# Kernel tuning notes

Hardware: AMD Instinct MI355X
Metric: run time of the kernel (lower is better)

## Reference

```python
import jax, jax.numpy as jnp
import numpy as np
from jax import lax


def _conv(x, w, b, pad):
    # x: [B,C,H,W], w: [O,I,kh,kw]
    y = lax.conv_general_dilated(x, w, (1, 1), [(pad, pad), (pad, pad)],
                                 dimension_numbers=('NCHW', 'OIHW', 'NCHW'))
    return y + b[None, :, None, None]


def _maxpool2(x):
    return lax.reduce_window(x, -jnp.inf, lax.max, (1, 1, 2, 2), (1, 1, 2, 2), 'VALID')


def setup_inputs() -> dict:
    key = jax.random.key(0)
    ks = jax.random.split(key, 6)
    N, T, R, D = 8, 64, 9, 512
    x = jax.random.normal(ks[0], (N, T, R, D), dtype=jnp.float32)
    x = x / jnp.linalg.norm(x, axis=-1, keepdims=True)  # ViSiL features are L2-normalized
    w1 = jax.random.normal(ks[1], (32, 1, 3, 3), dtype=jnp.float32) * 0.05
    w2 = jax.random.normal(ks[2], (64, 32, 3, 3), dtype=jnp.float32) * 0.05
    w3 = jax.random.normal(ks[3], (128, 64, 3, 3), dtype=jnp.float32) * 0.05
    w4 = jax.random.normal(ks[4], (1, 128, 1, 1), dtype=jnp.float32) * 0.05
    return {
        'x': x,
        'w1': w1, 'b1': jnp.zeros((32,), jnp.float32),
        'w2': w2, 'b2': jnp.zeros((64,), jnp.float32),
        'w3': w3, 'b3': jnp.zeros((128,), jnp.float32),
        'w4': w4, 'b4': jnp.zeros((1,), jnp.float32),
    }


def reference(x, w1, b1, w2, b2, w3, b3, w4, b4):
    N, T, R, D = x.shape
    # frame-to-frame similarity: region correlation volume + chamfer (max over p, mean over o)
    sim = jnp.einsum('aiok,bjpk->aiopjb', x, x)        # [a,i,o,p,j,b]
    sim = jnp.mean(jnp.max(sim, axis=3), axis=2)        # [a,i,j,b]
    sim = jnp.transpose(sim, (0, 3, 1, 2)).reshape(N * N, 1, T, T)  # '(a b) () i j'
    # VideoComparator CNN head (ZeroPad2d(1) + valid 3x3 conv == 'same' 3x3 conv)
    h = jax.nn.relu(_conv(sim, w1, b1, 1))
    h = _maxpool2(h)
    h = jax.nn.relu(_conv(h, w2, b2, 1))
    h = _maxpool2(h)
    h = jax.nn.relu(_conv(h, w3, b3, 1))
    h = _conv(h, w4, b4, 0)                              # [N*N, 1, T/4, T/4]
    # SimilarityRegularizationLoss(min_val=-1, max_val=1)
    loss = jnp.sum(jax.nn.relu(-(h + 1.0))) + jnp.sum(jax.nn.relu(h - 1.0))
    # Hardtanh, rescale to [0,1], then video-to-video chamfer
    s = jnp.clip(h, -1.0, 1.0) / 2.0 + 0.5
    s = jnp.mean(jnp.max(s, axis=3), axis=2)             # [N*N, 1]
    return s.reshape(N, N), loss
```

## Files before the change

### kernel.cpp

```cpp
#include <hip/hip_runtime.h>

typedef unsigned short u16;
typedef unsigned int u32;
typedef __bf16 bf16x8 __attribute__((ext_vector_type(8)));
typedef u16 u16x8 __attribute__((ext_vector_type(8)));
typedef float f32x4 __attribute__((ext_vector_type(4)));

__device__ __forceinline__ u16 f2bf(float f) {
  u32 u = __float_as_uint(f);
  u32 r = (u + 0x7FFFu + ((u >> 16) & 1u)) >> 16;
  return (u16)r;
}

__device__ __forceinline__ void gload16(const void* g, void* l) {
  typedef __attribute__((address_space(1))) const void gvoid;
  typedef __attribute__((address_space(3))) void lvoid;
  __builtin_amdgcn_global_load_lds((gvoid*)g, (lvoid*)l, 16, 0, 0);
}

__global__ void k_cast(const float* __restrict__ x, u16* __restrict__ A) {
  int t = blockIdx.x * 256 + threadIdx.x;
  const float4* xp = (const float4*)x + (size_t)t * 2;
  float4 v0 = xp[0], v1 = xp[1];
  u16x8 r;
  r[0] = f2bf(v0.x); r[1] = f2bf(v0.y); r[2] = f2bf(v0.z); r[3] = f2bf(v0.w);
  r[4] = f2bf(v1.x); r[5] = f2bf(v1.y); r[6] = f2bf(v1.z); r[7] = f2bf(v1.w);
  *(u16x8*)(A + (size_t)t * 8) = r;
}

__global__ __launch_bounds__(256) void k_gemm_smax(const u16* __restrict__ A,
                                                   float* __restrict__ Smax,
                                                   float* __restrict__ Sx) {
  __shared__ char smem[33536];
  const int rb = blockIdx.x, cb = blockIdx.y;
  if (rb > cb) return;
  u16* As = (u16*)smem;
  u16* Bs = (u16*)(smem + 16384);
  float* slab = (float*)smem;
  const int rowBase = rb * 128, colBase = cb * 128;
  const int tid = threadIdx.x, wave = tid >> 6, lane = tid & 63;
  const int lr = lane >> 3, lc = lane & 7;
  const int lrow = lane & 15, lk = lane >> 4;
  const int xr = lrow & 7;
  const int wr = (wave & 1) * 64, wc = (wave >> 1) * 64;

  f32x4 acc[4][4];
#pragma unroll
  for (int rt = 0; rt < 4; ++rt)
#pragma unroll
    for (int ct = 0; ct < 4; ++ct) { f32x4 z = {0.f, 0.f, 0.f, 0.f}; acc[rt][ct] = z; }

  for (int k0 = 0; k0 < 512; k0 += 64) {
    __syncthreads();
#pragma unroll
    for (int ii = 0; ii < 4; ++ii) {
      int r0 = wave * 32 + ii * 8;
      gload16(A + (size_t)(rowBase + r0 + lr) * 512 + k0 + ((lc ^ lr) * 8),
              As + r0 * 64);
      gload16(A + (size_t)(colBase + r0 + lr) * 512 + k0 + ((lc ^ lr) * 8),
              Bs + r0 * 64);
    }
    __syncthreads();
#pragma unroll
    for (int s = 0; s < 2; ++s) {
      bf16x8 af[4], bf[4];
#pragma unroll
      for (int rt = 0; rt < 4; ++rt)
        af[rt] = *(const bf16x8*)(As + (wr + rt * 16 + lrow) * 64 +
                                  ((u32)(s * 4 + lk) ^ xr) * 8);
#pragma unroll
      for (int ct = 0; ct < 4; ++ct)
        bf[ct] = *(const bf16x8*)(Bs + (wc + ct * 16 + lrow) * 64 +
                                  ((u32)(s * 4 + lk) ^ xr) * 8);
#pragma unroll
      for (int rt = 0; rt < 4; ++rt)
#pragma unroll
        for (int ct = 0; ct < 4; ++ct)
          acc[rt][ct] = __builtin_amdgcn_mfma_f32_16x16x32_bf16(af[rt], bf[ct],
                                                                acc[rt][ct], 0, 0, 0);
    }
  }

  const int g0c = colBase / 9, offc = colBase % 9;
  const int g0r = rowBase / 9, offr = rowBase % 9;
  const int nph = (rb == cb) ? 2 : 4;
  for (int ph = 0; ph < nph; ++ph) {
    __syncthreads();
    if (ph < 2) {
      if ((wave & 1) == ph) {
#pragma unroll
        for (int rt = 0; rt < 4; ++rt)
#pragma unroll
          for (int ct = 0; ct < 4; ++ct)
#pragma unroll
            for (int r = 0; r < 4; ++r)
              slab[(rt * 16 + lk * 4 + r) * 129 + wc + ct * 16 + lrow] = acc[rt][ct][r];
      }
    } else {
      if ((wave >> 1) == ph - 2) {
#pragma unroll
        for (int rt = 0; rt < 4; ++rt)
#pragma unroll
          for (int ct = 0; ct < 4; ++ct)
#pragma unroll
            for (int r = 0; r < 4; ++r)
              slab[(ct * 16 + lrow) * 129 + wr + rt * 16 + lk * 4 + r] = acc[rt][ct][r];
      }
    }
    __syncthreads();
    for (int it = tid; it < 1024; it += 256) {
      int line = it >> 4, s = it & 15;
      float m = -3.0e38f;
      if (ph < 2) {
        int g = g0c + s;
        int cs = 9 * g - colBase, ce = cs + 9;
        cs = cs < 0 ? 0 : cs;
        ce = ce > 128 ? 128 : ce;
        if (cs >= ce) continue;
        const float* p = slab + line * 129;
        for (int c = cs; c < ce; ++c) m = fmaxf(m, p[c]);
        int r = rowBase + ph * 64 + line;
        if (s == 0 && offc != 0) Sx[(size_t)r * 36 + (cb - 1)] = m;
        else Smax[(size_t)r * 512 + g] = m;
      } else {
        int g = g0r + s;
        int rs = 9 * g - rowBase, re = rs + 9;
        rs = rs < 0 ? 0 : rs;
        re = re > 128 ? 128 : re;
        if (rs >= re) continue;
        const float* p = slab + line * 129;
        for (int r2 = rs; r2 < re; ++r2) m = fmaxf(m, p[r2]);
        int cgl = colBase + (ph - 2) * 64 + line;
        if (s == 0 && offr != 0) Sx[(size_t)cgl * 36 + (rb - 1)] = m;
        else Smax[(size_t)cgl * 512 + g] = m;
      }
    }
  }
}

__global__ void k_reduce_o(const float* __restrict__ Smax, const float* __restrict__ Sx,
                           float* __restrict__ sim) {
  int idx = blockIdx.x * 256 + threadIdx.x;
  int j = idx & 63, i = (idx >> 6) & 63, b = (idx >> 12) & 7, a = idx >> 15;
  int g = b * 64 + j;
  int t9 = 9 * g;
  int k = (t9 + 8) >> 7;
  bool part = ((u32)(128 * k - t9 - 1) < 8u);
  const float* p = Smax + (size_t)(a * 576 + i * 9) * 512 + g;
  const float* q = Sx + (size_t)(a * 576 + i * 9) * 36 + (k - 1);
  float s = 0.f;
#pragma unroll
  for (int o = 0; o < 9; ++o) {
    float v = p[o * 512];
    if (part) v = fmaxf(v, q[o * 36]);
    s += v;
  }
  sim[idx] = s * (1.f / 9.f);
}

__global__ void k_wpack(const float* __restrict__ w2, const float* __restrict__ w3,
                        u16* __restrict__ p2, u16* __restrict__ p3,
                        float* __restrict__ out) {
  int i = blockIdx.x * 256 + threadIdx.x;
  if (blockIdx.x == 0 && threadIdx.x < 65) out[threadIdx.x] = 0.f;
  if (i < 18432) {
    int t = i >> 11, oc = (i >> 5) & 63, ic = i & 31;
    p2[i] = f2bf(w2[(oc * 32 + ic) * 9 + t]);
  }
  {
    int t = i >> 13, oc = (i >> 6) & 127, ic = i & 63;
    p3[i] = f2bf(w3[(oc * 64 + ic) * 9 + t]);
  }
}

__global__ __launch_bounds__(256) void k_conv1pool(const float* __restrict__ sim,
                                                   const float* __restrict__ w1,
                                                   const float* __restrict__ b1,
                                                   u16* __restrict__ h1) {
  __shared__ float tin[4096];
  const int pair = blockIdx.x, ocg = blockIdx.y, tid = threadIdx.x;
  const float4* src = (const float4*)(sim + (size_t)pair * 4096);
  for (int i = tid; i < 1024; i += 256) ((float4*)tin)[i] = src[i];
  __syncthreads();
  float wv[8][9], bs[8];
#pragma unroll
  for (int o = 0; o < 8; ++o) {
#pragma unroll
    for (int q = 0; q < 9; ++q) wv[o][q] = w1[(ocg * 8 + o) * 9 + q];
    bs[o] = b1[ocg * 8 + o];
  }
  for (int pp = tid; pp < 1024; pp += 256) {
    int py = pp >> 5, px = pp & 31;
    float m[8];
#pragma unroll
    for (int o = 0; o < 8; ++o) m[o] = 0.f;
#pragma unroll
    for (int dy = 0; dy < 2; ++dy)
#pragma unroll
      for (int dx = 0; dx < 2; ++dx) {
        float s[8];
#pragma unroll
        for (int o = 0; o < 8; ++o) s[o] = bs[o];
        int yy = py * 2 + dy, xx0 = px * 2 + dx;
#pragma unroll
        for (int ky = 0; ky < 3; ++ky) {
          int y = yy + ky - 1;
          if ((unsigned)y < 64u) {
#pragma unroll
            for (int kx = 0; kx < 3; ++kx) {
              int x = xx0 + kx - 1;
              if ((unsigned)x < 64u) {
                float v = tin[y * 64 + x];
#pragma unroll
                for (int o = 0; o < 8; ++o) s[o] += wv[o][ky * 3 + kx] * v;
              }
            }
          }
        }
#pragma unroll
        for (int o = 0; o < 8; ++o) m[o] = fmaxf(m[o], fmaxf(s[o], 0.f));
      }
    u16x8 r;
#pragma unroll
    for (int o = 0; o < 8; ++o) r[o] = f2bf(m[o]);
    *(u16x8*)&h1[(((size_t)pair * 32 + py) * 32 + px) * 32 + ocg * 8] = r;
  }
}

__global__ __launch_bounds__(256) void k_conv2pool(const u16* __restrict__ h1,
                                                   const u16* __restrict__ wp2,
                                                   const float* __restrict__ b2,
                                                   u16* __restrict__ h2) {
  __shared__ u16 tile[18 * 34 * 40];
  const int pair = blockIdx.x, yh = blockIdx.y, tid = threadIdx.x;
  const int wave = tid >> 6, lane = tid & 63, l15 = lane & 15, quad = lane >> 4;
  u16x8 z8 = {0, 0, 0, 0, 0, 0, 0, 0};
  for (int i = tid; i < 3060; i += 256) ((u16x8*)tile)[i] = z8;
  __syncthreads();
  for (int f = tid; f < 1152; f += 256) {
    int i = f >> 6, rem = f & 63, px = rem >> 1, half = rem & 1;
    int gr = yh * 16 - 1 + i;
    if ((unsigned)gr < 32u)
      *(u16x8*)&tile[(i * 34 + 1 + px) * 40 + half * 16] =
          *(const u16x8*)&h1[(((size_t)pair * 32 + gr) * 32 + px) * 32 + half * 16];
  }
  __syncthreads();

  f32x4 acc[8][4];
#pragma unroll
  for (int m = 0; m < 8; ++m)
#pragma unroll
    for (int n = 0; n < 4; ++n) { f32x4 z = {0.f, 0.f, 0.f, 0.f}; acc[m][n] = z; }

  for (int t = 0; t < 9; ++t) {
    int ky = t / 3, kx = t % 3;
    bf16x8 wf[4];
#pragma unroll
    for (int nt = 0; nt < 4; ++nt)
      wf[nt] = *(const bf16x8*)&wp2[((t * 64 + nt * 16 + l15) << 5) + quad * 8];
#pragma unroll
    for (int rr = 0; rr < 4; ++rr)
#pragma unroll
      for (int xh = 0; xh < 2; ++xh) {
        int lr = wave * 4 + rr;
        bf16x8 af = *(const bf16x8*)&tile[((lr + ky) * 34 + xh * 16 + l15 + kx) * 40 +
                                          quad * 8];
#pragma unroll
        for (int nt = 0; nt < 4; ++nt)
          acc[rr * 2 + xh][nt] =
              __builtin_amdgcn_mfma_f32_16x16x32_bf16(af, wf[nt], acc[rr * 2 + xh][nt],
                                                      0, 0, 0);
      }
  }

  float bv[4];
#pragma unroll
  for (int nt = 0; nt < 4; ++nt) bv[nt] = b2[nt * 16 + l15];
#pragma unroll
  for (int rp = 0; rp < 2; ++rp)
#pragma unroll
    for (int xh = 0; xh < 2; ++xh) {
      int py = yh * 8 + wave * 2 + rp;
      int px0 = xh * 8 + quad * 2;
#pragma unroll
      for (int nt = 0; nt < 4; ++nt) {
        f32x4 va = acc[(rp * 2) * 2 + xh][nt], vb = acc[(rp * 2 + 1) * 2 + xh][nt];
        float p0 = fmaxf(fmaxf(fmaxf(va[0], va[1]), fmaxf(vb[0], vb[1])) + bv[nt], 0.f);
        float p1 = fmaxf(fmaxf(fmaxf(va[2], va[3]), fmaxf(vb[2], vb[3])) + bv[nt], 0.f);
        size_t base = (((size_t)pair * 16 + py) * 16 + px0) * 64 + nt * 16 + l15;
        h2[base] = f2bf(p0);
        h2[base + 64] = f2bf(p1);
      }
    }
}

__global__ __launch_bounds__(256) void k_conv3(const u16* __restrict__ h2,
                                               const u16* __restrict__ wp3,
                                               const float* __restrict__ b3,
                                               float* __restrict__ h3) {
  __shared__ u16 tile[18 * 18 * 72];
  const int pair = blockIdx.x, oh = blockIdx.y, tid = threadIdx.x;
  const int wave = tid >> 6, lane = tid & 63, l15 = lane & 15, quad = lane >> 4;
  u16x8 z8 = {0, 0, 0, 0, 0, 0, 0, 0};
  for (int i = tid; i < 2916; i += 256) ((u16x8*)tile)[i] = z8;
  __syncthreads();
  for (int f = tid; f < 2048; f += 256) {
    int row = f >> 7, rem = f & 127, px = rem >> 3, seg = rem & 7;
    *(u16x8*)&tile[((row + 1) * 18 + px + 1) * 72 + seg * 8] =
        *(const u16x8*)&h2[(((size_t)pair * 16 + row) * 16 + px) * 64 + seg * 8];
  }
  __syncthreads();

  f32x4 acc[4][4];
#pragma unroll
  for (int m = 0; m < 4; ++m)
#pragma unroll
    for (int n = 0; n < 4; ++n) { f32x4 z = {0.f, 0.f, 0.f, 0.f}; acc[m][n] = z; }

  for (int t = 0; t < 9; ++t) {
    int ky = t / 3, kx = t % 3;
#pragma unroll
    for (int s = 0; s < 2; ++s) {
      bf16x8 wf[4];
#pragma unroll
      for (int nt = 0; nt < 4; ++nt)
        wf[nt] = *(const bf16x8*)&wp3[((t * 128 + oh * 64 + nt * 16 + l15) << 6) +
                                      s * 32 + quad * 8];
#pragma unroll
      for (int yt = 0; yt < 4; ++yt) {
        int y = wave * 4 + yt;
        bf16x8 af = *(const bf16x8*)&tile[((y + ky) * 18 + l15 + kx) * 72 + s * 32 +
                                          quad * 8];
#pragma unroll
        for (int nt = 0; nt < 4; ++nt)
          acc[yt][nt] = __builtin_amdgcn_mfma_f32_16x16x32_bf16(af, wf[nt],
                                                                acc[yt][nt], 0, 0, 0);
      }
    }
  }

  float bv[4];
#pragma unroll
  for (int nt = 0; nt < 4; ++nt) bv[nt] = b3[oh * 64 + nt * 16 + l15];
#pragma unroll
  for (int yt = 0; yt < 4; ++yt)
#pragma unroll
    for (int nt = 0; nt < 4; ++nt)
#pragma unroll
      for (int r = 0; r < 4; ++r) {
        int px = (wave * 4 + yt) * 16 + quad * 4 + r;
        h3[((size_t)pair * 256 + px) * 128 + oh * 64 + nt * 16 + l15] =
            fmaxf(acc[yt][nt][r] + bv[nt], 0.f);
      }
}

__global__ __launch_bounds__(256) void k_conv4(const float* __restrict__ h3,
                                               const float* __restrict__ w4,
                                               const float* __restrict__ b4,
                                               float* __restrict__ out) {
  __shared__ float ws4[128];
  __shared__ float rowmax[16];
  __shared__ float lsum[4];
  const int pair = blockIdx.x, tid = threadIdx.x;
  if (tid < 128) ws4[tid] = w4[tid];
  __syncthreads();
  float h = b4[0];
  const float4* p = (const float4*)(h3 + ((size_t)pair * 256 + tid) * 128);
#pragma unroll 8
  for (int i = 0; i < 32; ++i) {
    float4 v = p[i];
    h += v.x * ws4[i * 4] + v.y * ws4[i * 4 + 1] + v.z * ws4[i * 4 + 2] +
         v.w * ws4[i * 4 + 3];
  }
  float loss = fmaxf(-(h + 1.f), 0.f) + fmaxf(h - 1.f, 0.f);
  float sc = fminf(fmaxf(h, -1.f), 1.f) * 0.5f + 0.5f;
#pragma unroll
  for (int off = 8; off >= 1; off >>= 1) sc = fmaxf(sc, __shfl_xor(sc, off, 16));
#pragma unroll
  for (int off = 32; off >= 1; off >>= 1) loss += __shfl_xor(loss, off, 64);
  if ((tid & 15) == 0) rowmax[tid >> 4] = sc;
  if ((tid & 63) == 0) lsum[tid >> 6] = loss;
  __syncthreads();
  if (tid == 0) {
    float mean = 0.f;
#pragma unroll
    for (int i = 0; i < 16; ++i) mean += rowmax[i];
    out[pair] = mean * (1.f / 16.f);
    atomicAdd(out + 64, lsum[0] + lsum[1] + lsum[2] + lsum[3]);
  }
}

extern "C" void kernel_launch(void* const* d_in, const int* in_sizes, int n_in,
                              void* d_out, int out_size, void* d_ws, size_t ws_size,
                              hipStream_t stream) {
  (void)in_sizes; (void)n_in; (void)out_size; (void)ws_size;
  const float* x  = (const float*)d_in[0];
  const float* w1 = (const float*)d_in[1];
  const float* b1 = (const float*)d_in[2];
  const float* w2 = (const float*)d_in[3];
  const float* b2 = (const float*)d_in[4];
  const float* w3 = (const float*)d_in[5];
  const float* b3 = (const float*)d_in[6];
  const float* w4 = (const float*)d_in[7];
  const float* b4 = (const float*)d_in[8];
  float* out = (float*)d_out;

  char* ws = (char*)d_ws;
  u16*   Abf  = (u16*)ws;
  float* Smax = (float*)(ws + 4718592);
  float* Sx   = (float*)(ws + 14155776);
  float* sim  = (float*)(ws + 14819328);
  u16*   h1   = (u16*)(ws + 15867904);
  u16*   h2   = (u16*)(ws + 20062208);
  float* h3   = (float*)(ws + 22159360);
  u16*   wp2  = (u16*)(ws + 30547968);
  u16*   wp3  = (u16*)(ws + 30584832);

  k_cast<<<1152, 256, 0, stream>>>(x, Abf);
  k_gemm_smax<<<dim3(36, 36), 256, 0, stream>>>(Abf, Smax, Sx);
  k_wpack<<<288, 256, 0, stream>>>(w2, w3, wp2, wp3, out);
  k_reduce_o<<<1024, 256, 0, stream>>>(Smax, Sx, sim);
  k_conv1pool<<<dim3(64, 4), 256, 0, stream>>>(sim, w1, b1, h1);
  k_conv2pool<<<dim3(64, 2), 256, 0, stream>>>(h1, wp2, b2, h2);
  k_conv3<<<dim3(64, 2), 256, 0, stream>>>(h2, wp3, b3, h3);
  k_conv4<<<64, 256, 0, stream>>>(h3, w4, b4, out);
}
```

Before: 166.6 us.

## Double-buffer GEMM k-loop, launch only upper-triangle tiles, fuse weight packing into cast

The Gram GEMM now uses two shared-memory buffers: it issues the async global-to-LDS loads for the next k-slice while computing MFMAs on the current one, with one barrier per iteration. The grid becomes a 1D launch of the 666 upper-triangle tiles, with the tile index decoded by a sqrt plus correction loops, so the previously launched-then-exited lower-triangle blocks are gone. Weight packing and output zeroing move into the cast kernel, which removes one launch. Shared memory per block doubles to 64KB, which can lower occupancy.

```diff
diff --git a/kernel.cpp b/kernel.cpp
--- a/kernel.cpp
+++ b/kernel.cpp
@@ -18,7 +18,10 @@
   __builtin_amdgcn_global_load_lds((gvoid*)g, (lvoid*)l, 16, 0, 0);
 }
 
-__global__ void k_cast(const float* __restrict__ x, u16* __restrict__ A) {
+__global__ void k_cast(const float* __restrict__ x, u16* __restrict__ A,
+                       const float* __restrict__ w2, const float* __restrict__ w3,
+                       u16* __restrict__ p2, u16* __restrict__ p3,
+                       float* __restrict__ out) {
   int t = blockIdx.x * 256 + threadIdx.x;
   const float4* xp = (const float4*)x + (size_t)t * 2;
   float4 v0 = xp[0], v1 = xp[1];
@@ -26,17 +29,27 @@
   r[0] = f2bf(v0.x); r[1] = f2bf(v0.y); r[2] = f2bf(v0.z); r[3] = f2bf(v0.w);
   r[4] = f2bf(v1.x); r[5] = f2bf(v1.y); r[6] = f2bf(v1.z); r[7] = f2bf(v1.w);
   *(u16x8*)(A + (size_t)t * 8) = r;
+  if (blockIdx.x == 0 && threadIdx.x < 65) out[threadIdx.x] = 0.f;
+  if (t < 18432) {
+    int tt = t >> 11, oc = (t >> 5) & 63, ic = t & 31;
+    p2[t] = f2bf(w2[(oc * 32 + ic) * 9 + tt]);
+  }
+  if (t < 73728) {
+    int tt = t >> 13, oc = (t >> 6) & 127, ic = t & 63;
+    p3[t] = f2bf(w3[(oc * 64 + ic) * 9 + tt]);
+  }
 }
 
 __global__ __launch_bounds__(256) void k_gemm_smax(const u16* __restrict__ A,
                                                    float* __restrict__ Smax,
                                                    float* __restrict__ Sx) {
-  __shared__ char smem[33536];
-  const int rb = blockIdx.x, cb = blockIdx.y;
-  if (rb > cb) return;
-  u16* As = (u16*)smem;
-  u16* Bs = (u16*)(smem + 16384);
+  __shared__ char smem[65536];
   float* slab = (float*)smem;
+  const int tlin = blockIdx.x;
+  int rb = (int)((73.0f - sqrtf((float)(5329 - 8 * tlin))) * 0.5f);
+  while (rb * 36 - rb * (rb - 1) / 2 > tlin) --rb;
+  while ((rb + 1) * 36 - (rb + 1) * rb / 2 <= tlin) ++rb;
+  const int cb = rb + (tlin - (rb * 36 - rb * (rb - 1) / 2));
   const int rowBase = rb * 128, colBase = cb * 128;
   const int tid = threadIdx.x, wave = tid >> 6, lane = tid & 63;
   const int lr = lane >> 3, lc = lane & 7;
@@ -50,35 +63,56 @@
 #pragma unroll
     for (int ct = 0; ct < 4; ++ct) { f32x4 z = {0.f, 0.f, 0.f, 0.f}; acc[rt][ct] = z; }
 
-  for (int k0 = 0; k0 < 512; k0 += 64) {
-    __syncthreads();
+  {
+    u16* As = (u16*)smem;
+    u16* Bs = (u16*)(smem + 16384);
 #pragma unroll
     for (int ii = 0; ii < 4; ++ii) {
       int r0 = wave * 32 + ii * 8;
-      gload16(A + (size_t)(rowBase + r0 + lr) * 512 + k0 + ((lc ^ lr) * 8),
-              As + r0 * 64);
-      gload16(A + (size_t)(colBase + r0 + lr) * 512 + k0 + ((lc ^ lr) * 8),
-              Bs + r0 * 64);
+      gload16(A + (size_t)(rowBase + r0 + lr) * 512 + ((lc ^ lr) * 8), As + r0 * 64);
+      gload16(A + (size_t)(colBase + r0 + lr) * 512 + ((lc ^ lr) * 8), Bs + r0 * 64);
+    }
+  }
+  __syncthreads();
+  for (int k = 0; k < 8; ++k) {
+    if (k < 7) {
+      char* base = smem + (((k + 1) & 1) << 15);
+      u16* As = (u16*)base;
+      u16* Bs = (u16*)(base + 16384);
+      int k0 = (k + 1) * 64;
+#pragma unroll
+      for (int ii = 0; ii < 4; ++ii) {
+        int r0 = wave * 32 + ii * 8;
+        gload16(A + (size_t)(rowBase + r0 + lr) * 512 + k0 + ((lc ^ lr) * 8),
+                As + r0 * 64);
+        gload16(A + (size_t)(colBase + r0 + lr) * 512 + k0 + ((lc ^ lr) * 8),
+                Bs + r0 * 64);
+      }
+    }
+    {
+      char* base = smem + ((k & 1) << 15);
+      u16* As = (u16*)base;
+      u16* Bs = (u16*)(base + 16384);
+#pragma unroll
+      for (int s = 0; s < 2; ++s) {
+        bf16x8 af[4], bf[4];
+#pragma unroll
+        for (int rt = 0; rt < 4; ++rt)
+          af[rt] = *(const bf16x8*)(As + (wr + rt * 16 + lrow) * 64 +
+                                    ((u32)(s * 4 + lk) ^ xr) * 8);
+#pragma unroll
+        for (int ct = 0; ct < 4; ++ct)
+          bf[ct] = *(const bf16x8*)(Bs + (wc + ct * 16 + lrow) * 64 +
+                                    ((u32)(s * 4 + lk) ^ xr) * 8);
+#pragma unroll
+        for (int rt = 0; rt < 4; ++rt)
+#pragma unroll
+          for (int ct = 0; ct < 4; ++ct)
+            acc[rt][ct] = __builtin_amdgcn_mfma_f32_16x16x32_bf16(af[rt], bf[ct],
+                                                                  acc[rt][ct], 0, 0, 0);
+      }
     }
     __syncthreads();
-#pragma unroll
-    for (int s = 0; s < 2; ++s) {
-      bf16x8 af[4], bf[4];
-#pragma unroll
-      for (int rt = 0; rt < 4; ++rt)
-        af[rt] = *(const bf16x8*)(As + (wr + rt * 16 + lrow) * 64 +
-                                  ((u32)(s * 4 + lk) ^ xr) * 8);
-#pragma unroll
-      for (int ct = 0; ct < 4; ++ct)
-        bf[ct] = *(const bf16x8*)(Bs + (wc + ct * 16 + lrow) * 64 +
-                                  ((u32)(s * 4 + lk) ^ xr) * 8);
-#pragma unroll
-      for (int rt = 0; rt < 4; ++rt)
-#pragma unroll
-        for (int ct = 0; ct < 4; ++ct)
-          acc[rt][ct] = __builtin_amdgcn_mfma_f32_16x16x32_bf16(af[rt], bf[ct],
-                                                                acc[rt][ct], 0, 0, 0);
-    }
   }
 
   const int g0c = colBase / 9, offc = colBase % 9;
@@ -158,21 +192,6 @@
   sim[idx] = s * (1.f / 9.f);
 }
 
-__global__ void k_wpack(const float* __restrict__ w2, const float* __restrict__ w3,
-                        u16* __restrict__ p2, u16* __restrict__ p3,
-                        float* __restrict__ out) {
-  int i = blockIdx.x * 256 + threadIdx.x;
-  if (blockIdx.x == 0 && threadIdx.x < 65) out[threadIdx.x] = 0.f;
-  if (i < 18432) {
-    int t = i >> 11, oc = (i >> 5) & 63, ic = i & 31;
-    p2[i] = f2bf(w2[(oc * 32 + ic) * 9 + t]);
-  }
-  {
-    int t = i >> 13, oc = (i >> 6) & 127, ic = i & 63;
-    p3[i] = f2bf(w3[(oc * 64 + ic) * 9 + t]);
-  }
-}
-
 __global__ __launch_bounds__(256) void k_conv1pool(const float* __restrict__ sim,
                                                    const float* __restrict__ w1,
                                                    const float* __restrict__ b1,
@@ -416,9 +435,8 @@
   u16*   wp2  = (u16*)(ws + 30547968);
   u16*   wp3  = (u16*)(ws + 30584832);
 
-  k_cast<<<1152, 256, 0, stream>>>(x, Abf);
-  k_gemm_smax<<<dim3(36, 36), 256, 0, stream>>>(Abf, Smax, Sx);
-  k_wpack<<<288, 256, 0, stream>>>(w2, w3, wp2, wp3, out);
+  k_cast<<<1152, 256, 0, stream>>>(x, Abf, w2, w3, wp2, wp3, out);
+  k_gemm_smax<<<666, 256, 0, stream>>>(Abf, Smax, Sx);
   k_reduce_o<<<1024, 256, 0, stream>>>(Smax, Sx, sim);
   k_conv1pool<<<dim3(64, 4), 256, 0, stream>>>(sim, w1, b1, h1);
   k_conv2pool<<<dim3(64, 2), 256, 0, stream>>>(h1, wp2, b2, h2);
```

Result: faster. 161.1 us (-3.3%).
